# Kernel tuning notes

Hardware: AMD Instinct MI355X
Metric: run time of the kernel (lower is better)

The kernel has to match this reference:

```python
import jax, jax.numpy as jnp
import numpy as np
import math

B, T, N, D = 4, 12, 1024, 64
LN_EPS = 1e-5


def setup_inputs() -> dict:
    key = jax.random.key(0)
    k1, k2, k3 = jax.random.split(key, 3)
    X = jax.random.normal(k1, (B, T, N, D), dtype=jnp.float32)
    A = jax.random.uniform(k2, (N, N), dtype=jnp.float32)
    W = jax.random.normal(k3, (D, D), dtype=jnp.float32) * (1.0 / math.sqrt(D))
    gamma = jnp.ones((D,), dtype=jnp.float32)
    beta = jnp.zeros((D,), dtype=jnp.float32)
    return {"X": X, "A": A, "W": W, "gamma": gamma, "beta": beta}


def reference(X, A, W, gamma, beta):
    d = X.shape[-1]
    # dynamic attention scores: (b,t,n,m)
    scores = jnp.einsum('btnd,btmd->btnm', X, X)
    St = jax.nn.softmax(scores, axis=-1) / jnp.sqrt(jnp.float32(d)) + 1e-8
    # adjacency-gated dynamic graph: A (n,m) broadcast over (b,t)
    Ag = A[None, None, :, :] * St
    # graph conv: aggregate then linear (nn.Linear: H @ W.T), relu
    H = jnp.einsum('btnm,btmd->btnd', Ag, X)
    out = jax.nn.relu(H @ W.T)
    # layernorm over last dim
    mu = jnp.mean(out, axis=-1, keepdims=True)
    var = jnp.var(out, axis=-1, keepdims=True)
    out = (out - mu) * jax.lax.rsqrt(var + LN_EPS) * gamma + beta
    # residual
    return out + X
```

## Files before the change

### kernel.cpp

```cpp
#include <hip/hip_runtime.h>
#include <hip/hip_bf16.h>
#include <math.h>


typedef short bf16x8 __attribute__((ext_vector_type(8)));
typedef float f32x4  __attribute__((ext_vector_type(4)));
typedef float f32x16 __attribute__((ext_vector_type(16)));
typedef int   i32x4  __attribute__((ext_vector_type(4)));

constexpr int kN = 1024;
constexpr int kD = 64;
constexpr size_t kPlane    = 48u * 1024u * 64u;
constexpr size_t kAfShorts = 16u * 32u * 2048u;

#define MFMA32(a,b,c) __builtin_amdgcn_mfma_f32_32x32x16_bf16((a),(b),(c),0,0,0)
#define MFMA16(a,b,c) __builtin_amdgcn_mfma_f32_16x16x32_bf16((a),(b),(c),0,0,0)

__device__ __forceinline__ void splitv(float v, short& h, short& l) {
  unsigned u = __float_as_uint(v);
  h = (short)(u >> 16);
  float hf = __uint_as_float(u & 0xFFFF0000u);
  l = (short)(__float_as_uint(v - hf) >> 16);
}

__device__ __forceinline__ unsigned pkbf(float a, float b) {
  return (__float_as_uint(a) >> 16) | (__float_as_uint(b) & 0xFFFF0000u);
}

__global__ __launch_bounds__(256)
void presplit(const float* __restrict__ X, short* __restrict__ Xh,
              short* __restrict__ Xl, short* __restrict__ XTh)
{
  __shared__ short Sh[64][68], Sl[64][68];
  const int t  = threadIdx.x;
  const int bt = blockIdx.x >> 4;
  const int mb = blockIdx.x & 15;
  const size_t base = (size_t)bt * 65536 + (size_t)mb * 64 * 64;

#pragma unroll
  for (int k = 0; k < 4; ++k) {
    int idx = t + k * 256;
    int row = idx >> 4;
    int c4  = (idx & 15) * 4;
    float4 v = *(const float4*)(X + base + row * 64 + c4);
    short h0,l0,h1,l1,h2,l2,h3,l3;
    splitv(v.x, h0, l0); splitv(v.y, h1, l1);
    splitv(v.z, h2, l2); splitv(v.w, h3, l3);
    short4 hv = make_short4(h0, h1, h2, h3);
    short4 lv = make_short4(l0, l1, l2, l3);
    *(short4*)(Xh + base + row * 64 + c4) = hv;
    *(short4*)(Xl + base + row * 64 + c4) = lv;
    *(short4*)&Sh[row][c4] = hv;
    *(short4*)&Sl[row][c4] = lv;
  }
  __syncthreads();

  const size_t tbase = (size_t)bt * 65536 + (size_t)mb * 64;
#pragma unroll
  for (int k = 0; k < 2; ++k) {
    int idx = t + k * 256;
    int d   = idx >> 3;
    int m8  = (idx & 7) * 8;
    bf16x8 hv;
#pragma unroll
    for (int j = 0; j < 8; ++j) hv[j] = Sh[m8 + j][d];
    *(bf16x8*)(XTh + tbase + (size_t)d * 1024 + m8) = hv;
  }
}

__global__ __launch_bounds__(256)
void prearr_Abf(const float* __restrict__ A, short* __restrict__ Af)
{
  const int qt  = blockIdx.x >> 5;
  const int gks = blockIdx.x & 31;
  const int kb  = gks * 32;
  const int s   = threadIdx.x;
  short* dst = Af + ((size_t)(qt * 32 + gks) * 2048);

  const int qw = s >> 7;
  const int ln = (s >> 1) & 63;
  const int p  = s & 1;
  const int q  = qt * 64 + qw * 32 + (ln & 31);
  const int h  = ln >> 5;
  const int k0 = kb + 16 * p + 4 * h;
  float4 f0 = *(const float4*)(A + (size_t)q * kN + k0);
  float4 f1 = *(const float4*)(A + (size_t)q * kN + k0 + 8);
  i32x4 u;
  u[0] = (int)pkbf(f0.x, f0.y); u[1] = (int)pkbf(f0.z, f0.w);
  u[2] = (int)pkbf(f1.x, f1.y); u[3] = (int)pkbf(f1.z, f1.w);
  *(i32x4*)(dst + (size_t)qw * 1024 + ln * 16 + p * 8) = u;
}

template<int AMODE>
__global__ __launch_bounds__(256)
void sdgcn_v14(const float* __restrict__ X, const float* __restrict__ A,
               const float* __restrict__ W, const float* __restrict__ gamma,
               const float* __restrict__ beta, float* __restrict__ out,
               const short* __restrict__ Xh, const short* __restrict__ Xl,
               const short* __restrict__ XTh, const short* __restrict__ Af)
{
  __shared__ __align__(16) unsigned char LB[19456];

  const int t    = threadIdx.x;
  const int wave = t >> 6;
  const int lane = t & 63;
  const int kg   = wave >> 1;
  const int qw   = wave & 1;
  const int half = lane >> 5;
  const int l31  = lane & 31;
  const int bid  = blockIdx.x;
  const int swz  = (bid & 7) * 96 + (bid >> 3);
  const int bt   = swz >> 4;
  const int qt   = swz & 15;
  const int qblk = qt * 64;
  const size_t xb = (size_t)bt * 65536;

  short* Khg  = (short*)(LB + kg * 4608);
  short* Vthg = (short*)(LB + 9216 + kg * 5120);
  float* aM   = (float*)LB;
  float* aZ   = aM + 128;
  float* aF   = aZ + 128;
  float* Har  = (float*)(LB + 1792);

  const int qmine = qblk + qw * 32 + l31;
  bf16x8 qh[4], qlo[4];
#pragma unroll
  for (int c = 0; c < 4; ++c) {
    const size_t off = xb + (size_t)qmine * kD + 16 * c + half * 8;
    qh[c]  = *(const bf16x8*)(Xh + off);
    qlo[c] = *(const bf16x8*)(Xl + off);
  }

  f32x16 o0, o1;
#pragma unroll
  for (int r = 0; r < 16; ++r) { o0[r] = 0.f; o1[r] = 0.f; }
  float mrun = -INFINITY, Z = 0.f;

  const int tg = t & 127;

  auto ldK = [&](int kb, int j, bf16x8& h) {
    int ck = tg + 128 * j; int kr = ck >> 3; int kc = (ck & 7) * 8;
    h = *(const bf16x8*)(Xh + xb + (size_t)(kb + kr) * kD + kc);
  };
  auto ldV = [&](int kb, int j, bf16x8& h) {
    int cv = tg + 128 * j; int vd = cv >> 2; int vm = (cv & 3) * 8;
    h = *(const bf16x8*)(XTh + xb + (size_t)vd * 1024 + kb + vm);
  };
  auto stK = [&](int j, bf16x8 h) {
    int ck = tg + 128 * j; int kr = ck >> 3; int kc = (ck & 7) * 8;
    *(bf16x8*)&Khg[kr * 72 + kc] = h;
  };
  auto stV = [&](int j, bf16x8 h) {
    int cv = tg + 128 * j; int vd = cv >> 2; int vm = (cv & 3) * 8;
    *(bf16x8*)&Vthg[vd * 40 + vm] = h;
  };

  {
    bf16x8 a0,b0,c0,d0;
    ldK(kg * 512, 0, a0); ldK(kg * 512, 1, b0);
    ldV(kg * 512, 0, c0); ldV(kg * 512, 1, d0);
    stK(0, a0); stK(1, b0); stV(0, c0); stV(1, d0);
  }
  i32x4 aA = {0,0,0,0}, aB = {0,0,0,0};
  if (AMODE == 1) {
    const short* Ab = Af + ((size_t)(qt * 32 + kg * 16) * 2048)
                         + (size_t)qw * 1024 + (lane << 4);
    aA = *(const i32x4*)(Ab);
    aB = *(const i32x4*)(Ab + 8);
  }
  __syncthreads();

  for (int ks = 0; ks < 16; ++ks) {
    const int kb = kg * 512 + ks * 32;
    const bool pfm = (ks + 1) < 16;

    bf16x8 nk0,nk1,nv0,nv1;
    if (pfm) {
      ldK(kb + 32, 0, nk0); ldK(kb + 32, 1, nk1);
      ldV(kb + 32, 0, nv0); ldV(kb + 32, 1, nv1);
    }
    i32x4 naA = {0,0,0,0}, naB = {0,0,0,0};
    if (AMODE == 1 && pfm) {
      const short* Ab = Af + ((size_t)(qt * 32 + kg * 16 + ks + 1) * 2048)
                           + (size_t)qw * 1024 + (lane << 4);
      naA = *(const i32x4*)(Ab);
      naB = *(const i32x4*)(Ab + 8);
    }

    float agv[16];
    if (AMODE == 1) {
      unsigned u[8] = {(unsigned)aA[0],(unsigned)aA[1],(unsigned)aA[2],(unsigned)aA[3],
                       (unsigned)aB[0],(unsigned)aB[1],(unsigned)aB[2],(unsigned)aB[3]};
#pragma unroll
      for (int m = 0; m < 8; ++m) {
        agv[2*m]   = __uint_as_float(u[m] << 16);
        agv[2*m+1] = __uint_as_float(u[m] & 0xFFFF0000u);
      }
    } else {
      const float* Arow = A + (size_t)qmine * kN + kb + 4 * half;
      float4 ag0 = *(const float4*)(Arow);
      float4 ag1 = *(const float4*)(Arow + 8);
      float4 ag2 = *(const float4*)(Arow + 16);
      float4 ag3 = *(const float4*)(Arow + 24);
#pragma unroll
      for (int e = 0; e < 4; ++e) {
        agv[e] = ag0[e]; agv[4+e] = ag1[e]; agv[8+e] = ag2[e]; agv[12+e] = ag3[e];
      }
    }

    f32x16 sa;
#pragma unroll
    for (int r = 0; r < 16; ++r) sa[r] = 0.f;
    __builtin_amdgcn_s_setprio(1);
#pragma unroll
    for (int c = 0; c < 4; ++c) {
      bf16x8 kh = *(const bf16x8*)&Khg[l31 * 72 + 16 * c + half * 8];
      sa = MFMA32(kh, qh[c],  sa);
      sa = MFMA32(kh, qlo[c], sa);
    }
    __builtin_amdgcn_s_setprio(0);

    float a0 = fmaxf(fmaxf(sa[0],  sa[1]),  sa[2]);
    float a1 = fmaxf(fmaxf(sa[3],  sa[4]),  sa[5]);
    float a2 = fmaxf(fmaxf(sa[6],  sa[7]),  sa[8]);
    float a3 = fmaxf(fmaxf(sa[9],  sa[10]), sa[11]);
    float a4 = fmaxf(fmaxf(sa[12], sa[13]), sa[14]);
    float b0 = fmaxf(fmaxf(a0, a1), a2);
    float sm = fmaxf(fmaxf(b0, fmaxf(a3, a4)), sa[15]);
    sm = fmaxf(sm, __shfl_xor(sm, 32, 64));
    if (__any(sm > mrun + 8.f)) {
      const float nm = fmaxf(mrun, sm);
      const float f  = __expf(mrun - nm);
      mrun = nm; Z *= f;
#pragma unroll
      for (int r = 0; r < 16; ++r) {
        const float fr = __shfl(f, (r & 3) + 8 * (r >> 2) + 4 * half, 64);
        o0[r] *= fr; o1[r] *= fr;
      }
    }
    float pv[16];
#pragma unroll
    for (int r = 0; r < 16; ++r) pv[r] = __expf(sa[r] - mrun);
    float z0 = (pv[0] + pv[1]) + (pv[2] + pv[3]);
    float z1 = (pv[4] + pv[5]) + (pv[6] + pv[7]);
    float z2 = (pv[8] + pv[9]) + (pv[10] + pv[11]);
    float z3 = (pv[12] + pv[13]) + (pv[14] + pv[15]);
    float zt = (z0 + z1) + (z2 + z3);
    zt += __shfl_xor(zt, 32, 64);
    Z += zt;

    float pa[16];
#pragma unroll
    for (int r = 0; r < 16; ++r) pa[r] = pv[r] * agv[r];

    unsigned du[8];
#pragma unroll
    for (int j = 0; j < 8; ++j) du[j] = pkbf(pa[2*j], pa[2*j+1]);
    const bool lo = (half == 0);
    unsigned snd0 = lo ? du[2] : du[0];
    unsigned snd1 = lo ? du[3] : du[1];
    unsigned snd2 = lo ? du[6] : du[4];
    unsigned snd3 = lo ? du[7] : du[5];
    unsigned r0 = (unsigned)__shfl_xor((int)snd0, 32, 64);
    unsigned r1 = (unsigned)__shfl_xor((int)snd1, 32, 64);
    unsigned r2 = (unsigned)__shfl_xor((int)snd2, 32, 64);
    unsigned r3 = (unsigned)__shfl_xor((int)snd3, 32, 64);
    i32x4 w0, w1;
    w0[0] = (int)(lo ? du[0] : r0);
    w0[1] = (int)(lo ? du[1] : r1);
    w0[2] = (int)(lo ? r0 : du[2]);
    w0[3] = (int)(lo ? r1 : du[3]);
    w1[0] = (int)(lo ? du[4] : r2);
    w1[1] = (int)(lo ? du[5] : r3);
    w1[2] = (int)(lo ? r2 : du[6]);
    w1[3] = (int)(lo ? r3 : du[7]);
    bf16x8 pf0 = *(bf16x8*)&w0;
    bf16x8 pf1 = *(bf16x8*)&w1;

    {
      bf16x8 v0 = *(const bf16x8*)&Vthg[l31 * 40 + half * 8];
      bf16x8 v1 = *(const bf16x8*)&Vthg[l31 * 40 + 16 + half * 8];
      bf16x8 v2 = *(const bf16x8*)&Vthg[(32 + l31) * 40 + half * 8];
      bf16x8 v3 = *(const bf16x8*)&Vthg[(32 + l31) * 40 + 16 + half * 8];
      __builtin_amdgcn_s_setprio(1);
      o0 = MFMA32(pf0, v0, o0);
      o0 = MFMA32(pf1, v1, o0);
      o1 = MFMA32(pf0, v2, o1);
      o1 = MFMA32(pf1, v3, o1);
      __builtin_amdgcn_s_setprio(0);
    }

    __syncthreads();
    if (pfm) {
      stK(0, nk0); stK(1, nk1);
      stV(0, nv0); stV(1, nv1);
    }
    __syncthreads();
    aA = naA; aB = naB;
  }

  if (lane < 32) {
    aM[kg * 64 + qw * 32 + l31] = mrun;
    aZ[kg * 64 + qw * 32 + l31] = Z;
  }
  if (kg == 1) {
#pragma unroll
    for (int r = 0; r < 16; ++r) {
      const int qq = qw * 32 + (r & 3) + 8 * (r >> 2) + 4 * half;
      Har[qq * 68 + l31]      = o0[r];
      Har[qq * 68 + l31 + 32] = o1[r];
    }
  }
  __syncthreads();
  if (kg == 1 && lane < 32) {
    const int q = qw * 32 + l31;
    const float ma = aM[q], mb = mrun;
    const float m  = fmaxf(ma, mb);
    const float fa = __expf(ma - m), fb = __expf(mb - m);
    const float Zs = aZ[q] * fa + Z * fb;
    aF[q]       = fa;
    aF[64 + q]  = fb;
    aF[128 + q] = 1.0f / (8.0f * Zs);
  }
  __syncthreads();
  if (kg == 0) {
#pragma unroll
    for (int r = 0; r < 16; ++r) {
      const int qq = qw * 32 + (r & 3) + 8 * (r >> 2) + 4 * half;
      const float fa = aF[qq], fb = aF[64 + qq];
      Har[qq * 68 + l31]      = o0[r] * fa + Har[qq * 68 + l31]      * fb;
      Har[qq * 68 + l31 + 32] = o1[r] * fa + Har[qq * 68 + l31 + 32] * fb;
    }
  }
  __syncthreads();

  const int g  = lane >> 4;
  const int ql = lane & 15;
  const int er = wave * 16;
  const float i8z = aF[128 + er + ql];

  bf16x8 hh[2], hl[2];
#pragma unroll
  for (int kk = 0; kk < 2; ++kk) {
    const float* hp = &Har[(er + ql) * 68 + kk * 32 + g * 8];
    float4 v0 = *(const float4*)hp;
    float4 v1 = *(const float4*)(hp + 4);
    float v[8] = {v0.x*i8z, v0.y*i8z, v0.z*i8z, v0.w*i8z,
                  v1.x*i8z, v1.y*i8z, v1.z*i8z, v1.w*i8z};
#pragma unroll
    for (int e = 0; e < 8; ++e) { short a, b; splitv(v[e], a, b); hh[kk][e] = a; hl[kk][e] = b; }
  }

  f32x4 lin[4];
#pragma unroll
  for (int c = 0; c < 4; ++c) {
    bf16x8 wh[2], wl[2];
#pragma unroll
    for (int kk = 0; kk < 2; ++kk) {
      const float* wp = W + (size_t)(c * 16 + ql) * kD + kk * 32 + g * 8;
      float4 v0 = *(const float4*)wp;
      float4 v1 = *(const float4*)(wp + 4);
      float v[8] = {v0.x, v0.y, v0.z, v0.w, v1.x, v1.y, v1.z, v1.w};
#pragma unroll
      for (int e = 0; e < 8; ++e) { short a, b; splitv(v[e], a, b); wh[kk][e] = a; wl[kk][e] = b; }
    }
    f32x4 acc = {0.f, 0.f, 0.f, 0.f};
    acc = MFMA16(hh[0], wh[0], acc);
    acc = MFMA16(hh[1], wh[1], acc);
    acc = MFMA16(hh[0], wl[0], acc);
    acc = MFMA16(hh[1], wl[1], acc);
    acc = MFMA16(hl[0], wh[0], acc);
    acc = MFMA16(hl[1], wh[1], acc);
    lin[c] = acc;
  }

  float rl[4][4];
#pragma unroll
  for (int c = 0; c < 4; ++c)
#pragma unroll
    for (int r = 0; r < 4; ++r) rl[c][r] = fmaxf(lin[c][r], 0.f);

  float mu[4], rstd[4];
#pragma unroll
  for (int r = 0; r < 4; ++r) {
    float s1 = rl[0][r] + rl[1][r] + rl[2][r] + rl[3][r];
    float s2 = rl[0][r]*rl[0][r] + rl[1][r]*rl[1][r] + rl[2][r]*rl[2][r] + rl[3][r]*rl[3][r];
#pragma unroll
    for (int off = 1; off < 16; off <<= 1) {
      s1 += __shfl_xor(s1, off, 64);
      s2 += __shfl_xor(s2, off, 64);
    }
    mu[r] = s1 * (1.f / 64.f);
    const float var = s2 * (1.f / 64.f) - mu[r] * mu[r];
    rstd[r] = rsqrtf(var + 1e-5f);
  }

#pragma unroll
  for (int c = 0; c < 4; ++c) {
    const float gm = gamma[c * 16 + ql];
    const float bb = beta[c * 16 + ql];
#pragma unroll
    for (int r = 0; r < 4; ++r) {
      const int qrow = qblk + er + 4 * g + r;
      const size_t off = ((size_t)bt * kN + qrow) * kD + c * 16 + ql;
      out[off] = (rl[c][r] - mu[r]) * rstd[r] * gm + bb + X[off];
    }
  }
}

extern "C" void kernel_launch(void* const* d_in, const int* in_sizes, int n_in,
                              void* d_out, int out_size, void* d_ws, size_t ws_size,
                              hipStream_t stream) {
  const float* X     = (const float*)d_in[0];
  const float* A     = (const float*)d_in[1];
  const float* W     = (const float*)d_in[2];
  const float* gamma = (const float*)d_in[3];
  const float* beta  = (const float*)d_in[4];
  float* out = (float*)d_out;

  short* Xh  = (short*)d_ws;
  short* Xl  = Xh  + kPlane;
  short* XTh = Xl  + kPlane;
  short* Af  = XTh + kPlane;

  const size_t need = (3 * kPlane + kAfShorts) * sizeof(short);

  presplit<<<dim3(48 * 16), 256, 0, stream>>>(X, Xh, Xl, XTh);
  if (ws_size >= need) {
    prearr_Abf<<<dim3(16 * 32), 256, 0, stream>>>(A, Af);
    sdgcn_v14<1><<<dim3(48 * 16), 256, 0, stream>>>(X, A, W, gamma, beta, out,
                                                    Xh, Xl, XTh, Af);
  } else {
    sdgcn_v14<0><<<dim3(48 * 16), 256, 0, stream>>>(X, A, W, gamma, beta, out,
                                                    Xh, Xl, XTh, Af);
  }
}
```

Baseline: 65.48 us.

## Drop hi/lo bf16 split for scores and double-buffer K/V tiles in LDS

Replaces the two-term bf16 split of X with a single rounded bf16 copy, halving the QK^T MFMAs and removing the low-part plane from workspace and presplit. The main loop is restructured to ping-pong between two LDS buffers for K and V, so global loads for the next tile overlap compute and one barrier per step is removed. Softmax exponentials use exp2 with a pre-scaled log2e. The change trades score accuracy for speed, which may hurt fidelity given the large dot products, and doubles shared memory use.

```diff
diff --git a/kernel.cpp b/kernel.cpp
--- a/kernel.cpp
+++ b/kernel.cpp
@@ -12,6 +12,7 @@
 constexpr int kD = 64;
 constexpr size_t kPlane    = 48u * 1024u * 64u;
 constexpr size_t kAfShorts = 16u * 32u * 2048u;
+constexpr float  kLog2e    = 1.4426950408889634f;
 
 #define MFMA32(a,b,c) __builtin_amdgcn_mfma_f32_32x32x16_bf16((a),(b),(c),0,0,0)
 #define MFMA16(a,b,c) __builtin_amdgcn_mfma_f32_16x16x32_bf16((a),(b),(c),0,0,0)
@@ -23,15 +24,20 @@
   l = (short)(__float_as_uint(v - hf) >> 16);
 }
 
+__device__ __forceinline__ short rndbf(float v) {
+  unsigned u = __float_as_uint(v);
+  return (short)((u + 0x7FFFu + ((u >> 16) & 1u)) >> 16);
+}
+
 __device__ __forceinline__ unsigned pkbf(float a, float b) {
   return (__float_as_uint(a) >> 16) | (__float_as_uint(b) & 0xFFFF0000u);
 }
 
 __global__ __launch_bounds__(256)
 void presplit(const float* __restrict__ X, short* __restrict__ Xh,
-              short* __restrict__ Xl, short* __restrict__ XTh)
+              short* __restrict__ XTh)
 {
-  __shared__ short Sh[64][68], Sl[64][68];
+  __shared__ short Sh[64][68];
   const int t  = threadIdx.x;
   const int bt = blockIdx.x >> 4;
   const int mb = blockIdx.x & 15;
@@ -43,15 +49,9 @@
     int row = idx >> 4;
     int c4  = (idx & 15) * 4;
     float4 v = *(const float4*)(X + base + row * 64 + c4);
-    short h0,l0,h1,l1,h2,l2,h3,l3;
-    splitv(v.x, h0, l0); splitv(v.y, h1, l1);
-    splitv(v.z, h2, l2); splitv(v.w, h3, l3);
-    short4 hv = make_short4(h0, h1, h2, h3);
-    short4 lv = make_short4(l0, l1, l2, l3);
+    short4 hv = make_short4(rndbf(v.x), rndbf(v.y), rndbf(v.z), rndbf(v.w));
     *(short4*)(Xh + base + row * 64 + c4) = hv;
-    *(short4*)(Xl + base + row * 64 + c4) = lv;
     *(short4*)&Sh[row][c4] = hv;
-    *(short4*)&Sl[row][c4] = lv;
   }
   __syncthreads();
 
@@ -93,13 +93,13 @@
 
 template<int AMODE>
 __global__ __launch_bounds__(256)
-void sdgcn_v14(const float* __restrict__ X, const float* __restrict__ A,
+void sdgcn_v15(const float* __restrict__ X, const float* __restrict__ A,
                const float* __restrict__ W, const float* __restrict__ gamma,
                const float* __restrict__ beta, float* __restrict__ out,
-               const short* __restrict__ Xh, const short* __restrict__ Xl,
-               const short* __restrict__ XTh, const short* __restrict__ Af)
+               const short* __restrict__ Xh, const short* __restrict__ XTh,
+               const short* __restrict__ Af)
 {
-  __shared__ __align__(16) unsigned char LB[19456];
+  __shared__ __align__(16) unsigned char LB[38912];
 
   const int t    = threadIdx.x;
   const int wave = t >> 6;
@@ -115,21 +115,20 @@
   const int qblk = qt * 64;
   const size_t xb = (size_t)bt * 65536;
 
-  short* Khg  = (short*)(LB + kg * 4608);
-  short* Vthg = (short*)(LB + 9216 + kg * 5120);
-  float* aM   = (float*)LB;
-  float* aZ   = aM + 128;
-  float* aF   = aZ + 128;
-  float* Har  = (float*)(LB + 1792);
+  short* Kh0 = (short*)(LB + kg * 4608);
+  short* Kh1 = (short*)(LB + 9216 + kg * 4608);
+  short* Vt0 = (short*)(LB + 18432 + kg * 5120);
+  short* Vt1 = (short*)(LB + 28672 + kg * 5120);
+  float* aM  = (float*)LB;
+  float* aZ  = aM + 128;
+  float* aF  = aZ + 128;
+  float* Har = (float*)(LB + 1792);
 
   const int qmine = qblk + qw * 32 + l31;
-  bf16x8 qh[4], qlo[4];
-#pragma unroll
-  for (int c = 0; c < 4; ++c) {
-    const size_t off = xb + (size_t)qmine * kD + 16 * c + half * 8;
-    qh[c]  = *(const bf16x8*)(Xh + off);
-    qlo[c] = *(const bf16x8*)(Xl + off);
-  }
+  bf16x8 qh[4];
+#pragma unroll
+  for (int c = 0; c < 4; ++c)
+    qh[c] = *(const bf16x8*)(Xh + xb + (size_t)qmine * kD + 16 * c + half * 8);
 
   f32x16 o0, o1;
 #pragma unroll
@@ -146,41 +145,22 @@
     int cv = tg + 128 * j; int vd = cv >> 2; int vm = (cv & 3) * 8;
     h = *(const bf16x8*)(XTh + xb + (size_t)vd * 1024 + kb + vm);
   };
-  auto stK = [&](int j, bf16x8 h) {
+  auto stK = [&](short* Kh, int j, bf16x8 h) {
     int ck = tg + 128 * j; int kr = ck >> 3; int kc = (ck & 7) * 8;
-    *(bf16x8*)&Khg[kr * 72 + kc] = h;
+    *(bf16x8*)&Kh[kr * 72 + kc] = h;
   };
-  auto stV = [&](int j, bf16x8 h) {
+  auto stV = [&](short* Vt, int j, bf16x8 h) {
     int cv = tg + 128 * j; int vd = cv >> 2; int vm = (cv & 3) * 8;
-    *(bf16x8*)&Vthg[vd * 40 + vm] = h;
+    *(bf16x8*)&Vt[vd * 40 + vm] = h;
   };
 
-  {
-    bf16x8 a0,b0,c0,d0;
-    ldK(kg * 512, 0, a0); ldK(kg * 512, 1, b0);
-    ldV(kg * 512, 0, c0); ldV(kg * 512, 1, d0);
-    stK(0, a0); stK(1, b0); stV(0, c0); stV(1, d0);
-  }
   i32x4 aA = {0,0,0,0}, aB = {0,0,0,0};
-  if (AMODE == 1) {
-    const short* Ab = Af + ((size_t)(qt * 32 + kg * 16) * 2048)
-                         + (size_t)qw * 1024 + (lane << 4);
-    aA = *(const i32x4*)(Ab);
-    aB = *(const i32x4*)(Ab + 8);
-  }
-  __syncthreads();
-
-  for (int ks = 0; ks < 16; ++ks) {
+
+  auto compute = [&](int ks, const short* Khg, const short* Vtg, bool pfA) {
     const int kb = kg * 512 + ks * 32;
-    const bool pfm = (ks + 1) < 16;
-
-    bf16x8 nk0,nk1,nv0,nv1;
-    if (pfm) {
-      ldK(kb + 32, 0, nk0); ldK(kb + 32, 1, nk1);
-      ldV(kb + 32, 0, nv0); ldV(kb + 32, 1, nv1);
-    }
+
     i32x4 naA = {0,0,0,0}, naB = {0,0,0,0};
-    if (AMODE == 1 && pfm) {
+    if (AMODE == 1 && pfA) {
       const short* Ab = Af + ((size_t)(qt * 32 + kg * 16 + ks + 1) * 2048)
                            + (size_t)qw * 1024 + (lane << 4);
       naA = *(const i32x4*)(Ab);
@@ -215,8 +195,7 @@
 #pragma unroll
     for (int c = 0; c < 4; ++c) {
       bf16x8 kh = *(const bf16x8*)&Khg[l31 * 72 + 16 * c + half * 8];
-      sa = MFMA32(kh, qh[c],  sa);
-      sa = MFMA32(kh, qlo[c], sa);
+      sa = MFMA32(kh, qh[c], sa);
     }
     __builtin_amdgcn_s_setprio(0);
 
@@ -230,7 +209,7 @@
     sm = fmaxf(sm, __shfl_xor(sm, 32, 64));
     if (__any(sm > mrun + 8.f)) {
       const float nm = fmaxf(mrun, sm);
-      const float f  = __expf(mrun - nm);
+      const float f  = exp2f((mrun - nm) * kLog2e);
       mrun = nm; Z *= f;
 #pragma unroll
       for (int r = 0; r < 16; ++r) {
@@ -238,9 +217,10 @@
         o0[r] *= fr; o1[r] *= fr;
       }
     }
+    const float mb2 = mrun * kLog2e;
     float pv[16];
 #pragma unroll
-    for (int r = 0; r < 16; ++r) pv[r] = __expf(sa[r] - mrun);
+    for (int r = 0; r < 16; ++r) pv[r] = exp2f(fmaf(sa[r], kLog2e, -mb2));
     float z0 = (pv[0] + pv[1]) + (pv[2] + pv[3]);
     float z1 = (pv[4] + pv[5]) + (pv[6] + pv[7]);
     float z2 = (pv[8] + pv[9]) + (pv[10] + pv[11]);
@@ -278,10 +258,10 @@
     bf16x8 pf1 = *(bf16x8*)&w1;
 
     {
-      bf16x8 v0 = *(const bf16x8*)&Vthg[l31 * 40 + half * 8];
-      bf16x8 v1 = *(const bf16x8*)&Vthg[l31 * 40 + 16 + half * 8];
-      bf16x8 v2 = *(const bf16x8*)&Vthg[(32 + l31) * 40 + half * 8];
-      bf16x8 v3 = *(const bf16x8*)&Vthg[(32 + l31) * 40 + 16 + half * 8];
+      bf16x8 v0 = *(const bf16x8*)&Vtg[l31 * 40 + half * 8];
+      bf16x8 v1 = *(const bf16x8*)&Vtg[l31 * 40 + 16 + half * 8];
+      bf16x8 v2 = *(const bf16x8*)&Vtg[(32 + l31) * 40 + half * 8];
+      bf16x8 v3 = *(const bf16x8*)&Vtg[(32 + l31) * 40 + 16 + half * 8];
       __builtin_amdgcn_s_setprio(1);
       o0 = MFMA32(pf0, v0, o0);
       o0 = MFMA32(pf1, v1, o0);
@@ -289,14 +269,45 @@
       o1 = MFMA32(pf1, v3, o1);
       __builtin_amdgcn_s_setprio(0);
     }
-
+    aA = naA; aB = naB;
+  };
+
+  {
+    bf16x8 a0,b0,c0,d0;
+    ldK(kg * 512, 0, a0); ldK(kg * 512, 1, b0);
+    ldV(kg * 512, 0, c0); ldV(kg * 512, 1, d0);
+    stK(Kh0, 0, a0); stK(Kh0, 1, b0); stV(Vt0, 0, c0); stV(Vt0, 1, d0);
+  }
+  if (AMODE == 1) {
+    const short* Ab = Af + ((size_t)(qt * 32 + kg * 16) * 2048)
+                         + (size_t)qw * 1024 + (lane << 4);
+    aA = *(const i32x4*)(Ab);
+    aB = *(const i32x4*)(Ab + 8);
+  }
+  __syncthreads();
+
+  for (int ks = 0; ks < 16; ks += 2) {
+    bf16x8 k0,k1,v0,v1;
+    ldK(kg * 512 + (ks + 1) * 32, 0, k0);
+    ldK(kg * 512 + (ks + 1) * 32, 1, k1);
+    ldV(kg * 512 + (ks + 1) * 32, 0, v0);
+    ldV(kg * 512 + (ks + 1) * 32, 1, v1);
+    compute(ks, Kh0, Vt0, true);
+    stK(Kh1, 0, k0); stK(Kh1, 1, k1); stV(Vt1, 0, v0); stV(Vt1, 1, v1);
     __syncthreads();
-    if (pfm) {
-      stK(0, nk0); stK(1, nk1);
-      stV(0, nv0); stV(1, nv1);
+
+    const bool more = (ks + 2) < 16;
+    if (more) {
+      ldK(kg * 512 + (ks + 2) * 32, 0, k0);
+      ldK(kg * 512 + (ks + 2) * 32, 1, k1);
+      ldV(kg * 512 + (ks + 2) * 32, 0, v0);
+      ldV(kg * 512 + (ks + 2) * 32, 1, v1);
+    }
+    compute(ks + 1, Kh1, Vt1, more);
+    if (more) {
+      stK(Kh0, 0, k0); stK(Kh0, 1, k1); stV(Vt0, 0, v0); stV(Vt0, 1, v1);
     }
     __syncthreads();
-    aA = naA; aB = naB;
   }
 
   if (lane < 32) {
@@ -419,19 +430,18 @@
   float* out = (float*)d_out;
 
   short* Xh  = (short*)d_ws;
-  short* Xl  = Xh  + kPlane;
-  short* XTh = Xl  + kPlane;
+  short* XTh = Xh  + kPlane;
   short* Af  = XTh + kPlane;
 
-  const size_t need = (3 * kPlane + kAfShorts) * sizeof(short);
-
-  presplit<<<dim3(48 * 16), 256, 0, stream>>>(X, Xh, Xl, XTh);
+  const size_t need = (2 * kPlane + kAfShorts) * sizeof(short);
+
+  presplit<<<dim3(48 * 16), 256, 0, stream>>>(X, Xh, XTh);
   if (ws_size >= need) {
     prearr_Abf<<<dim3(16 * 32), 256, 0, stream>>>(A, Af);
-    sdgcn_v14<1><<<dim3(48 * 16), 256, 0, stream>>>(X, A, W, gamma, beta, out,
-                                                    Xh, Xl, XTh, Af);
+    sdgcn_v15<1><<<dim3(48 * 16), 256, 0, stream>>>(X, A, W, gamma, beta, out,
+                                                    Xh, XTh, Af);
   } else {
-    sdgcn_v14<0><<<dim3(48 * 16), 256, 0, stream>>>(X, A, W, gamma, beta, out,
-                                                    Xh, Xl, XTh, Af);
-  }
-}
+    sdgcn_v15<0><<<dim3(48 * 16), 256, 0, stream>>>(X, A, W, gamma, beta, out,
+                                                    Xh, XTh, Af);
+  }
+}
```

New measurement: 63.65 us. 2.8% less time.
